# Kernel optimization log

Hardware: AMD Instinct MI355X
Metric: run time of the kernel (lower is better)

## Reference

```python
import jax, jax.numpy as jnp
import numpy as np

B, T, D, HS = 4, 2048, 1024, 64

def setup_inputs() -> dict:
    key = jax.random.key(0)
    kx, kk, kq, kv = jax.random.split(key, 4)
    scale = 1.0 / np.sqrt(D)
    return {
        "x": jax.random.normal(kx, (B, T, D), dtype=jnp.float32),
        "Wk": jax.random.normal(kk, (D, HS), dtype=jnp.float32) * scale,
        "Wq": jax.random.normal(kq, (D, HS), dtype=jnp.float32) * scale,
        "Wv": jax.random.normal(kv, (D, HS), dtype=jnp.float32) * scale,
    }

def reference(x, Wk, Wq, Wv):
    # x: [B, T, D]; projections to [B, T, HS]
    k = jnp.einsum("btd,dh->bth", x, Wk)
    q = jnp.einsum("btd,dh->bth", x, Wq)
    v = jnp.einsum("btd,dh->bth", x, Wv)
    # scores [B, T, T]; NOTE: original multiplies by sqrt(head_size) (faithful)
    att = jnp.einsum("bth,bsh->bts", q, k) * jnp.sqrt(jnp.float32(k.shape[-1]))
    Tq = x.shape[1]
    causal = jnp.tril(jnp.ones((Tq, Tq), dtype=bool))
    att = jnp.where(causal[None, :, :], att, -jnp.inf)
    p = jax.nn.softmax(att, axis=-1)
    # dropout = identity (eval mode)
    return jnp.einsum("bts,bsh->bth", p, v)
```

## Files before the change

### kernel.cpp

```cpp
#include <hip/hip_runtime.h>

#define Bn 4
#define Tn 2048
#define Dn 1024
#define HSn 64

typedef __attribute__((ext_vector_type(8))) short bf16x8;
typedef __attribute__((ext_vector_type(4))) float f32x4;
typedef __attribute__((ext_vector_type(4))) short s16x4;
typedef unsigned short u16;
typedef unsigned int u32;

__device__ __forceinline__ u16 f2bf_rne(float x) {
    u32 u = __float_as_uint(x);
    return (u16)((u + 0x7FFFu + ((u >> 16) & 1u)) >> 16);
}
__device__ __forceinline__ u16 f2bf_trunc(float x) {
    return (u16)(__float_as_uint(x) >> 16);
}
__device__ __forceinline__ float bf2f(u16 h) {
    return __uint_as_float(((u32)h) << 16);
}

#define GLL16(g, l)                                                        \
    __builtin_amdgcn_global_load_lds(                                      \
        (const __attribute__((address_space(1))) void*)(g),                \
        (__attribute__((address_space(3))) void*)(l), 16, 0, 0)

__global__ __launch_bounds__(256) void wprep_kernel(
    const float* __restrict__ Wk, const float* __restrict__ Wq,
    const float* __restrict__ Wv, u16* __restrict__ wtp)
{
    __shared__ float ws_[64][65];
    const int kb = blockIdx.x;
    const int w  = blockIdx.y;
    const float* __restrict__ W = (w == 0) ? Wk : (w == 1) ? Wq : Wv;
    const float scale = (w == 1) ? 8.0f : 1.0f;
    const int t = threadIdx.x;

    {
        const int kl = t >> 2, hq = t & 3;
        #pragma unroll
        for (int i = 0; i < 4; ++i) {
            float4 f = *(const float4*)(W + (size_t)(kb * 64 + kl) * 64 + hq * 16 + i * 4);
            ws_[kl][hq * 16 + i * 4 + 0] = f.x; ws_[kl][hq * 16 + i * 4 + 1] = f.y;
            ws_[kl][hq * 16 + i * 4 + 2] = f.z; ws_[kl][hq * 16 + i * 4 + 3] = f.w;
        }
    }
    __syncthreads();

    const int h = t & 63, quarter = t >> 6;
    const int n = w * 64 + h;
    const int ks = kb * 2 + (quarter >> 1);
    const int k_in0 = (quarter & 1) * 16;
    u16 hib[16], lob[16];
    #pragma unroll
    for (int j = 0; j < 16; ++j) {
        float v = ws_[quarter * 16 + j][h] * scale;
        u16 hi = f2bf_trunc(v);
        hib[j] = hi;
        lob[j] = f2bf_trunc(v - bf2f(hi));
    }
    u16* dst = wtp + (size_t)n * 2048 + ks * 64;
    *(uint4*)(dst + k_in0)          = *(const uint4*)&hib[0];
    *(uint4*)(dst + k_in0 + 8)      = *(const uint4*)&hib[8];
    *(uint4*)(dst + 32 + k_in0)     = *(const uint4*)&lob[0];
    *(uint4*)(dst + 32 + k_in0 + 8) = *(const uint4*)&lob[8];
}

#define NKS 32
#define XB(P) (smem + (P) * 4096)
#define BB(P) (smem + 12288 + (P) * 12288)

__global__ __launch_bounds__(256) void proj_gemm(
    const float* __restrict__ x, const u16* __restrict__ wtp,
    u16* __restrict__ qh8, u16* __restrict__ ql8,
    u16* __restrict__ kth, u16* __restrict__ ktl,
    u16* __restrict__ vtt)
{
    __shared__ __align__(16) unsigned char smem[49152];

    const int tid  = threadIdx.x;
    const int wave = tid >> 6, lane = tid & 63;
    const int lo4  = lane & 15, g = lane >> 4;
    const int ch   = blockIdx.x >> 8;
    const int row0 = (blockIdx.x & 255) * 32;
    const int rt   = wave >> 1;
    const int cbase = (wave & 1) * 3;
    const int rl = rt * 16 + lo4;
    const int wcol0 = ch * 96;

    f32x4 acc[3];
    #pragma unroll
    for (int c = 0; c < 3; ++c) acc[c] = (f32x4){0.f, 0.f, 0.f, 0.f};

    const int xr = tid >> 3, xc = tid & 7;
    const int xsw = (xc ^ (xr & 7)) << 2;
    const float* xsrc0 = x + (size_t)(row0 + xr) * Dn + xsw;

    #define STAGE(P, KS)                                                     \
        {                                                                    \
            GLL16(xsrc0 + (KS) * 32, XB(P) + tid * 16);                      \
            _Pragma("unroll")                                                \
            for (int i = 0; i < 3; ++i) {                                    \
                const int c = i * 256 + tid;                                 \
                const int n_ = c >> 3, p_ = c & 7;                           \
                const int l_ = p_ ^ (n_ & 7);                                \
                const u16* src = wtp + (size_t)(wcol0 + n_) * 2048 + (KS) * 64 \
                                 + ((l_ & 3) << 3) + ((l_ >> 2) << 5);       \
                GLL16(src, BB(P) + c * 16);                                  \
            }                                                                \
        }

    #define COMPUTE(P, KS)                                                   \
        {                                                                    \
            bf16x8 ah, al;                                                   \
            {                                                                \
                const unsigned char* xb = XB(P) + rl * 128;                  \
                f32x4 f0 = *(const f32x4*)(xb + (((2 * g + 0) ^ (rl & 7)) << 4)); \
                f32x4 f1 = *(const f32x4*)(xb + (((2 * g + 1) ^ (rl & 7)) << 4)); \
                _Pragma("unroll")                                            \
                for (int jj = 0; jj < 4; ++jj) {                             \
                    u16 h0 = f2bf_trunc(f0[jj]);                             \
                    ah[jj] = (short)h0;                                      \
                    al[jj] = (short)f2bf_trunc(f0[jj] - bf2f(h0));           \
                    u16 h1 = f2bf_trunc(f1[jj]);                             \
                    ah[4 + jj] = (short)h1;                                  \
                    al[4 + jj] = (short)f2bf_trunc(f1[jj] - bf2f(h1));       \
                }                                                            \
            }                                                                \
            _Pragma("unroll")                                                \
            for (int ct = 0; ct < 3; ++ct) {                                 \
                const int n = (cbase + ct) * 16 + lo4;                       \
                const unsigned char* bb = BB(P) + n * 128;                   \
                bf16x8 bh = *(const bf16x8*)(bb + (((g)     ^ (n & 7)) << 4)); \
                bf16x8 bl = *(const bf16x8*)(bb + (((4 + g) ^ (n & 7)) << 4)); \
                acc[ct] = __builtin_amdgcn_mfma_f32_16x16x32_bf16(ah, bh, acc[ct], 0, 0, 0); \
                acc[ct] = __builtin_amdgcn_mfma_f32_16x16x32_bf16(al, bh, acc[ct], 0, 0, 0); \
                acc[ct] = __builtin_amdgcn_mfma_f32_16x16x32_bf16(ah, bl, acc[ct], 0, 0, 0); \
            }                                                                \
        }

    STAGE(0, 0)
    STAGE(1, 1)
    int pb = 0;
    for (int ks = 0; ks < NKS; ++ks) {
        if (ks == NKS - 1) {
            asm volatile("s_waitcnt vmcnt(0)" ::: "memory");
        } else {
            asm volatile("s_waitcnt vmcnt(4)" ::: "memory");
        }
        __builtin_amdgcn_s_barrier();
        asm volatile("" ::: "memory");

        int ps = pb + 2; if (ps >= 3) ps -= 3;
        if (ks + 2 < NKS) STAGE(ps, ks + 2)
        COMPUTE(pb, ks)
        pb = (pb == 2) ? 0 : pb + 1;
    }

    const int grow = row0 + rt * 16 + g * 4;
    const int bb_ = grow >> 11, tl = grow & 2047;
    #pragma unroll
    for (int ct = 0; ct < 3; ++ct) {
        const int n = wcol0 + (cbase + ct) * 16 + lo4;
        if (n < 64) {
            const int kch = n >> 5, gi = (n >> 3) & 3, e = n & 7;
            const size_t base = (size_t)bb_ * 131072
                + (size_t)(((((tl >> 4) * 2 + kch) * 4 + gi) * 16 + (tl & 15)) * 8 + e);
            #pragma unroll
            for (int reg = 0; reg < 4; ++reg) {
                float v = acc[ct][reg];
                u16 hi = f2bf_trunc(v);
                kth[base + reg * 8] = hi;
                ktl[base + reg * 8] = f2bf_trunc(v - bf2f(hi));
            }
        } else if (n < 128) {
            #pragma unroll
            for (int reg = 0; reg < 4; ++reg) {
                float v = acc[ct][reg];
                u16 hi = f2bf_trunc(v);
                qh8[(size_t)(grow + reg) * HSn + (n - 64)] = hi;
                ql8[(size_t)(grow + reg) * HSn + (n - 64)] = f2bf_trunc(v - bf2f(hi));
            }
        } else {
            const int h = n - 128;
            s16x4 pack;
            #pragma unroll
            for (int reg = 0; reg < 4; ++reg)
                pack[reg] = (short)f2bf_rne(acc[ct][reg]);
            const size_t vidx = (size_t)bb_ * 131072
                + (size_t)((tl >> 5) * 2048 + (h >> 4) * 512 + (h & 15) * 32
                           + ((tl >> 3) & 3) * 8 + (tl & 7));
            *(s16x4*)(vtt + vidx) = pack;
        }
    }
}

struct KVset {
    bf16x8 kh0[2], kh1[2], kl0[2], kl1[2], vf[4];
};

__global__ __launch_bounds__(256, 2) void attn_kernel(
    const u16* __restrict__ qh8, const u16* __restrict__ ql8,
    const u16* __restrict__ kth, const u16* __restrict__ ktl,
    const u16* __restrict__ vtt, float* __restrict__ out)
{
    __shared__ __align__(16) unsigned char pbuf[4096];
    __shared__ __align__(16) float om_s[4][16][64];
    __shared__ float ml_s[4][16][2];

    const int tid  = threadIdx.x;
    const int wave = tid >> 6, lane = tid & 63;
    const int lo4  = lane & 15, g = lane >> 4;

    const int sblk = blockIdx.x >> 8, c = blockIdx.x & 255;
    const int tb = sblk ? 127 - (c >> 1) : (c >> 1);
    const int b  = 2 * sblk + (c & 1);
    const int t0 = tb * 16;

    const u16* qhp = qh8 + ((size_t)b * Tn + t0) * HSn;
    const u16* qlp = ql8 + ((size_t)b * Tn + t0) * HSn;
    const u16* kthb = kth + (size_t)b * 131072;
    const u16* ktlb = ktl + (size_t)b * 131072;
    const u16* vttb = vtt + (size_t)b * 131072;
    const int klane = lane * 8;
    const int vlane = lo4 * 32 + g * 8;

    bf16x8 qfh[2], qfl[2];
    #pragma unroll
    for (int ch = 0; ch < 2; ++ch) {
        qfh[ch] = *(const bf16x8*)(qhp + lo4 * HSn + ch * 32 + g * 8);
        qfl[ch] = *(const bf16x8*)(qlp + lo4 * HSn + ch * 32 + g * 8);
    }

    bf16x8 vones;
    #pragma unroll
    for (int i = 0; i < 8; ++i) vones[i] = (short)0x3F80;

    f32x4 O[4];
    #pragma unroll
    for (int n = 0; n < 4; ++n) O[n] = (f32x4){0.f, 0.f, 0.f, 0.f};
    float mrow[4], lrow[4];
    #pragma unroll
    for (int r = 0; r < 4; ++r) { mrow[r] = -1e30f; lrow[r] = 0.f; }

    const int nt = (t0 + 15) / 32 + 1;
    unsigned char* myPB = pbuf + wave * 1024;

    #define LOADSET(S, J)                                                     \
        {                                                                     \
            const u16* kb_ = kthb + (size_t)(2 * (J)) * 1024 + klane;         \
            const u16* lb_ = ktlb + (size_t)(2 * (J)) * 1024 + klane;         \
            S.kh0[0] = *(const bf16x8*)(kb_);                                 \
            S.kh1[0] = *(const bf16x8*)(kb_ + 512);                           \
            S.kh0[1] = *(const bf16x8*)(kb_ + 1024);                          \
            S.kh1[1] = *(const bf16x8*)(kb_ + 1536);                          \
            S.kl0[0] = *(const bf16x8*)(lb_);                                 \
            S.kl1[0] = *(const bf16x8*)(lb_ + 512);                           \
            S.kl0[1] = *(const bf16x8*)(lb_ + 1024);                          \
            S.kl1[1] = *(const bf16x8*)(lb_ + 1536);                          \
            const u16* vb_ = vttb + (size_t)(J) * 2048 + vlane;               \
            S.vf[0] = *(const bf16x8*)(vb_);                                  \
            S.vf[1] = *(const bf16x8*)(vb_ + 512);                            \
            S.vf[2] = *(const bf16x8*)(vb_ + 1024);                           \
            S.vf[3] = *(const bf16x8*)(vb_ + 1536);                           \
        }

    #define COMPUTE_ATT(S, J)                                                 \
        {                                                                     \
            const int s0 = (J) * 32;                                          \
            f32x4 accS[2];                                                    \
            __builtin_amdgcn_s_setprio(1);                                    \
            _Pragma("unroll")                                                 \
            for (int sb = 0; sb < 2; ++sb) {                                  \
                f32x4 a = (f32x4){0.f, 0.f, 0.f, 0.f};                        \
                a = __builtin_amdgcn_mfma_f32_16x16x32_bf16(qfh[0], S.kh0[sb], a, 0, 0, 0); \
                a = __builtin_amdgcn_mfma_f32_16x16x32_bf16(qfh[1], S.kh1[sb], a, 0, 0, 0); \
                a = __builtin_amdgcn_mfma_f32_16x16x32_bf16(qfl[0], S.kh0[sb], a, 0, 0, 0); \
                a = __builtin_amdgcn_mfma_f32_16x16x32_bf16(qfl[1], S.kh1[sb], a, 0, 0, 0); \
                a = __builtin_amdgcn_mfma_f32_16x16x32_bf16(qfh[0], S.kl0[sb], a, 0, 0, 0); \
                a = __builtin_amdgcn_mfma_f32_16x16x32_bf16(qfh[1], S.kl1[sb], a, 0, 0, 0); \
                accS[sb] = a;                                                 \
            }                                                                 \
            __builtin_amdgcn_s_setprio(0);                                    \
            float v0s[4], v1s[4], mts[4];                                     \
            _Pragma("unroll")                                                 \
            for (int reg = 0; reg < 4; ++reg) {                               \
                const int tg  = t0 + g * 4 + reg;                             \
                v0s[reg] = (s0 + lo4      <= tg) ? accS[0][reg] : -1e30f;     \
                v1s[reg] = (s0 + 16 + lo4 <= tg) ? accS[1][reg] : -1e30f;     \
                float mt = fmaxf(v0s[reg], v1s[reg]);                         \
                mt = fmaxf(mt, __shfl_xor(mt, 1));                            \
                mt = fmaxf(mt, __shfl_xor(mt, 2));                            \
                mt = fmaxf(mt, __shfl_xor(mt, 4));                            \
                mt = fmaxf(mt, __shfl_xor(mt, 8));                            \
                mts[reg] = mt;                                                \
            }                                                                 \
            const bool grew = (mts[0] > mrow[0]) | (mts[1] > mrow[1])         \
                            | (mts[2] > mrow[2]) | (mts[3] > mrow[3]);        \
            if (__any(grew)) {                                                \
                _Pragma("unroll")                                             \
                for (int reg = 0; reg < 4; ++reg) {                           \
                    float mn = fmaxf(mrow[reg], mts[reg]);                    \
                    float alpha = __expf(mrow[reg] - mn);                     \
                    lrow[reg] *= alpha;                                       \
                    mrow[reg] = mn;                                           \
                    _Pragma("unroll")                                         \
                    for (int n = 0; n < 4; ++n) O[n][reg] *= alpha;           \
                }                                                             \
            }                                                                 \
            _Pragma("unroll")                                                 \
            for (int reg = 0; reg < 4; ++reg) {                               \
                const int tg  = t0 + g * 4 + reg;                             \
                float p0 = (s0 + lo4      <= tg) ? __expf(v0s[reg] - mrow[reg]) : 0.f; \
                float p1 = (s0 + 16 + lo4 <= tg) ? __expf(v1s[reg] - mrow[reg]) : 0.f; \
                const int irow = g * 4 + reg;                                 \
                *(u16*)(myPB + ((irow * 64 + lo4 * 2) ^ (reg << 4)))      = f2bf_rne(p0); \
                *(u16*)(myPB + ((irow * 64 + 32 + lo4 * 2) ^ (reg << 4))) = f2bf_rne(p1); \
            }                                                                 \
            bf16x8 pf = *(const bf16x8*)(myPB + ((lo4 * 64 + 16 * g) ^ ((lo4 & 3) << 4))); \
            __builtin_amdgcn_s_setprio(1);                                    \
            f32x4 lacc = (f32x4){0.f, 0.f, 0.f, 0.f};                         \
            lacc = __builtin_amdgcn_mfma_f32_16x16x32_bf16(pf, vones, lacc, 0, 0, 0); \
            _Pragma("unroll")                                                 \
            for (int n = 0; n < 4; ++n)                                       \
                O[n] = __builtin_amdgcn_mfma_f32_16x16x32_bf16(pf, S.vf[n], O[n], 0, 0, 0); \
            __builtin_amdgcn_s_setprio(0);                                    \
            _Pragma("unroll")                                                 \
            for (int reg = 0; reg < 4; ++reg) lrow[reg] += lacc[reg];         \
        }

    KVset A, B;
    int j = wave;
    if (j < nt) LOADSET(A, j)
    while (j < nt) {
        if (j + 4 < nt) LOADSET(B, j + 4)
        COMPUTE_ATT(A, j)
        if (j + 4 < nt) {
            if (j + 8 < nt) LOADSET(A, j + 8)
            COMPUTE_ATT(B, j + 4)
        }
        j += 8;
    }

    #pragma unroll
    for (int n = 0; n < 4; ++n)
        #pragma unroll
        for (int reg = 0; reg < 4; ++reg)
            om_s[wave][g * 4 + reg][n * 16 + lo4] = O[n][reg];
    if (lo4 == 0) {
        #pragma unroll
        for (int reg = 0; reg < 4; ++reg) {
            ml_s[wave][g * 4 + reg][0] = mrow[reg];
            ml_s[wave][g * 4 + reg][1] = lrow[reg];
        }
    }
    __syncthreads();

    const int r  = tid >> 4;
    const int h4 = (tid & 15) * 4;
    float mw[4], lw[4], mstar = -1e30f;
    #pragma unroll
    for (int w = 0; w < 4; ++w) {
        mw[w] = ml_s[w][r][0];
        lw[w] = ml_s[w][r][1];
        mstar = fmaxf(mstar, mw[w]);
    }
    float lstar = 0.f, ew[4];
    #pragma unroll
    for (int w = 0; w < 4; ++w) { ew[w] = __expf(mw[w] - mstar); lstar += lw[w] * ew[w]; }
    float4 a4 = {0.f, 0.f, 0.f, 0.f};
    #pragma unroll
    for (int w = 0; w < 4; ++w) {
        float4 t4 = *(const float4*)&om_s[w][r][h4];
        a4.x += t4.x * ew[w]; a4.y += t4.y * ew[w];
        a4.z += t4.z * ew[w]; a4.w += t4.w * ew[w];
    }
    const float inv = 1.f / lstar;
    a4.x *= inv; a4.y *= inv; a4.z *= inv; a4.w *= inv;
    *(float4*)(out + ((size_t)b * Tn + t0 + r) * HSn + h4) = a4;
}

extern "C" void kernel_launch(void* const* d_in, const int* in_sizes, int n_in,
                              void* d_out, int out_size, void* d_ws, size_t ws_size,
                              hipStream_t stream) {
    const float* x  = (const float*)d_in[0];
    const float* Wk = (const float*)d_in[1];
    const float* Wq = (const float*)d_in[2];
    const float* Wv = (const float*)d_in[3];
    float* out = (float*)d_out;

    const size_t per = (size_t)Bn * Tn * HSn;
    u16* qh8 = (u16*)d_ws;
    u16* ql8 = qh8 + per;
    u16* kth = ql8 + per;
    u16* ktl = kth + per;
    u16* vtt = ktl + per;
    u16* wtp = vtt + per;

    hipLaunchKernelGGL(wprep_kernel, dim3(16, 3), dim3(256), 0, stream,
                       Wk, Wq, Wv, wtp);
    hipLaunchKernelGGL(proj_gemm, dim3(512), dim3(256), 0, stream,
                       x, wtp, qh8, ql8, kth, ktl, vtt);
    hipLaunchKernelGGL(attn_kernel, dim3(512), dim3(256), 0, stream,
                       qh8, ql8, kth, ktl, vtt, out);
}
```

Baseline: 45.88 us.

## Compute all projection columns per block to reuse converted x tiles

Each proj_gemm block now covers all 192 Q/K/V output columns for its 32 rows instead of half of them, so the grid shrinks from 512 to 256 blocks. Each wave handles both 16-row subtiles across three column tiles, reusing the hi/lo bf16 conversion of x and the loaded weight fragments. This avoids loading and splitting each x tile twice, at the cost of a much larger LDS footprint (weights buffer doubled), more accumulator registers, and fewer blocks for latency hiding.

```diff
diff --git a/kernel.cpp b/kernel.cpp
--- a/kernel.cpp
+++ b/kernel.cpp
@@ -70,7 +70,7 @@
 
 #define NKS 32
 #define XB(P) (smem + (P) * 4096)
-#define BB(P) (smem + 12288 + (P) * 12288)
+#define BB(P) (smem + 12288 + (P) * 24576)
 
 __global__ __launch_bounds__(256) void proj_gemm(
     const float* __restrict__ x, const u16* __restrict__ wtp,
@@ -78,21 +78,19 @@
     u16* __restrict__ kth, u16* __restrict__ ktl,
     u16* __restrict__ vtt)
 {
-    __shared__ __align__(16) unsigned char smem[49152];
+    __shared__ __align__(16) unsigned char smem[86016];
 
     const int tid  = threadIdx.x;
     const int wave = tid >> 6, lane = tid & 63;
     const int lo4  = lane & 15, g = lane >> 4;
-    const int ch   = blockIdx.x >> 8;
-    const int row0 = (blockIdx.x & 255) * 32;
-    const int rt   = wave >> 1;
-    const int cbase = (wave & 1) * 3;
-    const int rl = rt * 16 + lo4;
-    const int wcol0 = ch * 96;
-
-    f32x4 acc[3];
-    #pragma unroll
-    for (int c = 0; c < 3; ++c) acc[c] = (f32x4){0.f, 0.f, 0.f, 0.f};
+    const int row0 = blockIdx.x * 32;
+    const int cbase = wave * 3;
+
+    f32x4 acc[2][3];
+    #pragma unroll
+    for (int r2 = 0; r2 < 2; ++r2)
+        #pragma unroll
+        for (int c = 0; c < 3; ++c) acc[r2][c] = (f32x4){0.f, 0.f, 0.f, 0.f};
 
     const int xr = tid >> 3, xc = tid & 7;
     const int xsw = (xc ^ (xr & 7)) << 2;
@@ -102,11 +100,11 @@
         {                                                                    \
             GLL16(xsrc0 + (KS) * 32, XB(P) + tid * 16);                      \
             _Pragma("unroll")                                                \
-            for (int i = 0; i < 3; ++i) {                                    \
+            for (int i = 0; i < 6; ++i) {                                    \
                 const int c = i * 256 + tid;                                 \
                 const int n_ = c >> 3, p_ = c & 7;                           \
                 const int l_ = p_ ^ (n_ & 7);                                \
-                const u16* src = wtp + (size_t)(wcol0 + n_) * 2048 + (KS) * 64 \
+                const u16* src = wtp + (size_t)n_ * 2048 + (KS) * 64         \
                                  + ((l_ & 3) << 3) + ((l_ >> 2) << 5);       \
                 GLL16(src, BB(P) + c * 16);                                  \
             }                                                                \
@@ -114,19 +112,21 @@
 
     #define COMPUTE(P, KS)                                                   \
         {                                                                    \
-            bf16x8 ah, al;                                                   \
-            {                                                                \
-                const unsigned char* xb = XB(P) + rl * 128;                  \
-                f32x4 f0 = *(const f32x4*)(xb + (((2 * g + 0) ^ (rl & 7)) << 4)); \
-                f32x4 f1 = *(const f32x4*)(xb + (((2 * g + 1) ^ (rl & 7)) << 4)); \
+            bf16x8 ah[2], al[2];                                             \
+            _Pragma("unroll")                                                \
+            for (int r2 = 0; r2 < 2; ++r2) {                                 \
+                const int rl2 = r2 * 16 + lo4;                               \
+                const unsigned char* xb = XB(P) + rl2 * 128;                 \
+                f32x4 f0 = *(const f32x4*)(xb + (((2 * g + 0) ^ (rl2 & 7)) << 4)); \
+                f32x4 f1 = *(const f32x4*)(xb + (((2 * g + 1) ^ (rl2 & 7)) << 4)); \
                 _Pragma("unroll")                                            \
                 for (int jj = 0; jj < 4; ++jj) {                             \
                     u16 h0 = f2bf_trunc(f0[jj]);                             \
-                    ah[jj] = (short)h0;                                      \
-                    al[jj] = (short)f2bf_trunc(f0[jj] - bf2f(h0));           \
+                    ah[r2][jj] = (short)h0;                                  \
+                    al[r2][jj] = (short)f2bf_trunc(f0[jj] - bf2f(h0));       \
                     u16 h1 = f2bf_trunc(f1[jj]);                             \
-                    ah[4 + jj] = (short)h1;                                  \
-                    al[4 + jj] = (short)f2bf_trunc(f1[jj] - bf2f(h1));       \
+                    ah[r2][4 + jj] = (short)h1;                              \
+                    al[r2][4 + jj] = (short)f2bf_trunc(f1[jj] - bf2f(h1));   \
                 }                                                            \
             }                                                                \
             _Pragma("unroll")                                                \
@@ -135,9 +135,12 @@
                 const unsigned char* bb = BB(P) + n * 128;                   \
                 bf16x8 bh = *(const bf16x8*)(bb + (((g)     ^ (n & 7)) << 4)); \
                 bf16x8 bl = *(const bf16x8*)(bb + (((4 + g) ^ (n & 7)) << 4)); \
-                acc[ct] = __builtin_amdgcn_mfma_f32_16x16x32_bf16(ah, bh, acc[ct], 0, 0, 0); \
-                acc[ct] = __builtin_amdgcn_mfma_f32_16x16x32_bf16(al, bh, acc[ct], 0, 0, 0); \
-                acc[ct] = __builtin_amdgcn_mfma_f32_16x16x32_bf16(ah, bl, acc[ct], 0, 0, 0); \
+                _Pragma("unroll")                                            \
+                for (int r2 = 0; r2 < 2; ++r2) {                             \
+                    acc[r2][ct] = __builtin_amdgcn_mfma_f32_16x16x32_bf16(ah[r2], bh, acc[r2][ct], 0, 0, 0); \
+                    acc[r2][ct] = __builtin_amdgcn_mfma_f32_16x16x32_bf16(al[r2], bh, acc[r2][ct], 0, 0, 0); \
+                    acc[r2][ct] = __builtin_amdgcn_mfma_f32_16x16x32_bf16(ah[r2], bl, acc[r2][ct], 0, 0, 0); \
+                }                                                            \
             }                                                                \
         }
 
@@ -148,7 +151,7 @@
         if (ks == NKS - 1) {
             asm volatile("s_waitcnt vmcnt(0)" ::: "memory");
         } else {
-            asm volatile("s_waitcnt vmcnt(4)" ::: "memory");
+            asm volatile("s_waitcnt vmcnt(7)" ::: "memory");
         }
         __builtin_amdgcn_s_barrier();
         asm volatile("" ::: "memory");
@@ -159,40 +162,43 @@
         pb = (pb == 2) ? 0 : pb + 1;
     }
 
-    const int grow = row0 + rt * 16 + g * 4;
-    const int bb_ = grow >> 11, tl = grow & 2047;
-    #pragma unroll
-    for (int ct = 0; ct < 3; ++ct) {
-        const int n = wcol0 + (cbase + ct) * 16 + lo4;
-        if (n < 64) {
-            const int kch = n >> 5, gi = (n >> 3) & 3, e = n & 7;
-            const size_t base = (size_t)bb_ * 131072
-                + (size_t)(((((tl >> 4) * 2 + kch) * 4 + gi) * 16 + (tl & 15)) * 8 + e);
-            #pragma unroll
-            for (int reg = 0; reg < 4; ++reg) {
-                float v = acc[ct][reg];
-                u16 hi = f2bf_trunc(v);
-                kth[base + reg * 8] = hi;
-                ktl[base + reg * 8] = f2bf_trunc(v - bf2f(hi));
+    #pragma unroll
+    for (int r2 = 0; r2 < 2; ++r2) {
+        const int grow = row0 + r2 * 16 + g * 4;
+        const int bb_ = grow >> 11, tl = grow & 2047;
+        #pragma unroll
+        for (int ct = 0; ct < 3; ++ct) {
+            const int n = (cbase + ct) * 16 + lo4;
+            if (n < 64) {
+                const int kch = n >> 5, gi = (n >> 3) & 3, e = n & 7;
+                const size_t base = (size_t)bb_ * 131072
+                    + (size_t)(((((tl >> 4) * 2 + kch) * 4 + gi) * 16 + (tl & 15)) * 8 + e);
+                #pragma unroll
+                for (int reg = 0; reg < 4; ++reg) {
+                    float v = acc[r2][ct][reg];
+                    u16 hi = f2bf_trunc(v);
+                    kth[base + reg * 8] = hi;
+                    ktl[base + reg * 8] = f2bf_trunc(v - bf2f(hi));
+                }
+            } else if (n < 128) {
+                #pragma unroll
+                for (int reg = 0; reg < 4; ++reg) {
+                    float v = acc[r2][ct][reg];
+                    u16 hi = f2bf_trunc(v);
+                    qh8[(size_t)(grow + reg) * HSn + (n - 64)] = hi;
+                    ql8[(size_t)(grow + reg) * HSn + (n - 64)] = f2bf_trunc(v - bf2f(hi));
+                }
+            } else {
+                const int h = n - 128;
+                s16x4 pack;
+                #pragma unroll
+                for (int reg = 0; reg < 4; ++reg)
+                    pack[reg] = (short)f2bf_rne(acc[r2][ct][reg]);
+                const size_t vidx = (size_t)bb_ * 131072
+                    + (size_t)((tl >> 5) * 2048 + (h >> 4) * 512 + (h & 15) * 32
+                               + ((tl >> 3) & 3) * 8 + (tl & 7));
+                *(s16x4*)(vtt + vidx) = pack;
             }
-        } else if (n < 128) {
-            #pragma unroll
-            for (int reg = 0; reg < 4; ++reg) {
-                float v = acc[ct][reg];
-                u16 hi = f2bf_trunc(v);
-                qh8[(size_t)(grow + reg) * HSn + (n - 64)] = hi;
-                ql8[(size_t)(grow + reg) * HSn + (n - 64)] = f2bf_trunc(v - bf2f(hi));
-            }
-        } else {
-            const int h = n - 128;
-            s16x4 pack;
-            #pragma unroll
-            for (int reg = 0; reg < 4; ++reg)
-                pack[reg] = (short)f2bf_rne(acc[ct][reg]);
-            const size_t vidx = (size_t)bb_ * 131072
-                + (size_t)((tl >> 5) * 2048 + (h >> 4) * 512 + (h & 15) * 32
-                           + ((tl >> 3) & 3) * 8 + (tl & 7));
-            *(s16x4*)(vtt + vidx) = pack;
         }
     }
 }
@@ -401,7 +407,7 @@
 
     hipLaunchKernelGGL(wprep_kernel, dim3(16, 3), dim3(256), 0, stream,
                        Wk, Wq, Wv, wtp);
-    hipLaunchKernelGGL(proj_gemm, dim3(512), dim3(256), 0, stream,
+    hipLaunchKernelGGL(proj_gemm, dim3(256), dim3(256), 0, stream,
                        x, wtp, qh8, ql8, kth, ktl, vtt);
     hipLaunchKernelGGL(attn_kernel, dim3(512), dim3(256), 0, stream,
                        qh8, ql8, kth, ktl, vtt, out);
```

After: 50.51 us. 1.1x slower.

## Pre-swizzle weights into MFMA fragment layout and load them directly to registers

Applied to the files above, without the earlier changes.

The weight-prep kernel now writes the bf16 hi/lo weights already arranged in per-lane MFMA fragment order. The projection GEMM reads these fragments straight from global memory into registers, double-buffered across k-steps, instead of staging them through LDS. x is now staged in larger 128-wide chunks with one barrier per chunk rather than one per 32-wide step, and MFMA issue is wrapped in s_setprio. This cuts LDS traffic and barrier count, at the cost of more register pressure and global-load latency that is exposed unless the register prefetch hides it.

```diff
diff --git a/kernel.cpp b/kernel.cpp
--- a/kernel.cpp
+++ b/kernel.cpp
@@ -29,7 +29,7 @@
 
 __global__ __launch_bounds__(256) void wprep_kernel(
     const float* __restrict__ Wk, const float* __restrict__ Wq,
-    const float* __restrict__ Wv, u16* __restrict__ wtp)
+    const float* __restrict__ Wv, u16* __restrict__ wtp2)
 {
     __shared__ float ws_[64][65];
     const int kb = blockIdx.x;
@@ -50,9 +50,8 @@
     __syncthreads();
 
     const int h = t & 63, quarter = t >> 6;
-    const int n = w * 64 + h;
-    const int ks = kb * 2 + (quarter >> 1);
-    const int k_in0 = (quarter & 1) * 16;
+    const int nt = w * 4 + (h >> 4);
+    const int ksub = quarter >> 1;
     u16 hib[16], lob[16];
     #pragma unroll
     for (int j = 0; j < 16; ++j) {
@@ -61,34 +60,35 @@
         hib[j] = hi;
         lob[j] = f2bf_trunc(v - bf2f(hi));
     }
-    u16* dst = wtp + (size_t)n * 2048 + ks * 64;
-    *(uint4*)(dst + k_in0)          = *(const uint4*)&hib[0];
-    *(uint4*)(dst + k_in0 + 8)      = *(const uint4*)&hib[8];
-    *(uint4*)(dst + 32 + k_in0)     = *(const uint4*)&lob[0];
-    *(uint4*)(dst + 32 + k_in0 + 8) = *(const uint4*)&lob[8];
-}
-
-#define NKS 32
-#define XB(P) (smem + (P) * 4096)
-#define BB(P) (smem + 12288 + (P) * 12288)
+    const int lane0 = ((quarter * 2 + 0) & 3) * 16 + (h & 15);
+    const int lane1 = ((quarter * 2 + 1) & 3) * 16 + (h & 15);
+    u16* base = wtp2 + (size_t)kb * 24576 + (size_t)(ksub * 12 + nt) * 1024;
+    *(uint4*)(base + lane0 * 8)       = *(const uint4*)&hib[0];
+    *(uint4*)(base + lane1 * 8)       = *(const uint4*)&hib[8];
+    *(uint4*)(base + 512 + lane0 * 8) = *(const uint4*)&lob[0];
+    *(uint4*)(base + 512 + lane1 * 8) = *(const uint4*)&lob[8];
+}
+
+struct Bset { bf16x8 bh[3], bl[3]; };
 
 __global__ __launch_bounds__(256) void proj_gemm(
-    const float* __restrict__ x, const u16* __restrict__ wtp,
+    const float* __restrict__ x, const u16* __restrict__ wtp2,
     u16* __restrict__ qh8, u16* __restrict__ ql8,
     u16* __restrict__ kth, u16* __restrict__ ktl,
     u16* __restrict__ vtt)
 {
-    __shared__ __align__(16) unsigned char smem[49152];
+    __shared__ __align__(16) unsigned char smem[32768];
 
     const int tid  = threadIdx.x;
     const int wave = tid >> 6, lane = tid & 63;
     const int lo4  = lane & 15, g = lane >> 4;
-    const int ch   = blockIdx.x >> 8;
+    const int chh  = blockIdx.x >> 8;
     const int row0 = (blockIdx.x & 255) * 32;
     const int rt   = wave >> 1;
-    const int cbase = (wave & 1) * 3;
-    const int rl = rt * 16 + lo4;
-    const int wcol0 = ch * 96;
+    const int cg   = wave & 1;
+    const int rl   = rt * 16 + lo4;
+    const int wcol0 = chh * 96;
+    const int ntbase = chh * 6 + cg * 3;
 
     f32x4 acc[3];
     #pragma unroll
@@ -97,73 +97,75 @@
     const int xr = tid >> 3, xc = tid & 7;
     const int xsw = (xc ^ (xr & 7)) << 2;
     const float* xsrc0 = x + (size_t)(row0 + xr) * Dn + xsw;
-
-    #define STAGE(P, KS)                                                     \
+    const u16* bp0 = wtp2 + (size_t)ntbase * 1024 + lane * 8;
+
+    #define XSTAGE(P, W_)                                                    \
         {                                                                    \
-            GLL16(xsrc0 + (KS) * 32, XB(P) + tid * 16);                      \
             _Pragma("unroll")                                                \
-            for (int i = 0; i < 3; ++i) {                                    \
-                const int c = i * 256 + tid;                                 \
-                const int n_ = c >> 3, p_ = c & 7;                           \
-                const int l_ = p_ ^ (n_ & 7);                                \
-                const u16* src = wtp + (size_t)(wcol0 + n_) * 2048 + (KS) * 64 \
-                                 + ((l_ & 3) << 3) + ((l_ >> 2) << 5);       \
-                GLL16(src, BB(P) + c * 16);                                  \
-            }                                                                \
-        }
-
-    #define COMPUTE(P, KS)                                                   \
+            for (int s_ = 0; s_ < 4; ++s_)                                   \
+                GLL16(xsrc0 + (W_) * 128 + s_ * 32,                          \
+                      smem + (P) * 16384 + s_ * 4096 + tid * 16);            \
+        }
+
+    #define LOADB(S, KS)                                                     \
         {                                                                    \
-            bf16x8 ah, al;                                                   \
-            {                                                                \
-                const unsigned char* xb = XB(P) + rl * 128;                  \
-                f32x4 f0 = *(const f32x4*)(xb + (((2 * g + 0) ^ (rl & 7)) << 4)); \
-                f32x4 f1 = *(const f32x4*)(xb + (((2 * g + 1) ^ (rl & 7)) << 4)); \
-                _Pragma("unroll")                                            \
-                for (int jj = 0; jj < 4; ++jj) {                             \
-                    u16 h0 = f2bf_trunc(f0[jj]);                             \
-                    ah[jj] = (short)h0;                                      \
-                    al[jj] = (short)f2bf_trunc(f0[jj] - bf2f(h0));           \
-                    u16 h1 = f2bf_trunc(f1[jj]);                             \
-                    ah[4 + jj] = (short)h1;                                  \
-                    al[4 + jj] = (short)f2bf_trunc(f1[jj] - bf2f(h1));       \
-                }                                                            \
-            }                                                                \
+            const u16* bp = bp0 + (size_t)(KS) * 12288;                      \
             _Pragma("unroll")                                                \
             for (int ct = 0; ct < 3; ++ct) {                                 \
-                const int n = (cbase + ct) * 16 + lo4;                       \
-                const unsigned char* bb = BB(P) + n * 128;                   \
-                bf16x8 bh = *(const bf16x8*)(bb + (((g)     ^ (n & 7)) << 4)); \
-                bf16x8 bl = *(const bf16x8*)(bb + (((4 + g) ^ (n & 7)) << 4)); \
-                acc[ct] = __builtin_amdgcn_mfma_f32_16x16x32_bf16(ah, bh, acc[ct], 0, 0, 0); \
-                acc[ct] = __builtin_amdgcn_mfma_f32_16x16x32_bf16(al, bh, acc[ct], 0, 0, 0); \
-                acc[ct] = __builtin_amdgcn_mfma_f32_16x16x32_bf16(ah, bl, acc[ct], 0, 0, 0); \
+                S.bh[ct] = *(const bf16x8*)(bp + ct * 1024);                 \
+                S.bl[ct] = *(const bf16x8*)(bp + ct * 1024 + 512);           \
             }                                                                \
         }
 
-    STAGE(0, 0)
-    STAGE(1, 1)
-    int pb = 0;
-    for (int ks = 0; ks < NKS; ++ks) {
-        if (ks == NKS - 1) {
-            asm volatile("s_waitcnt vmcnt(0)" ::: "memory");
-        } else {
-            asm volatile("s_waitcnt vmcnt(4)" ::: "memory");
-        }
-        __builtin_amdgcn_s_barrier();
-        asm volatile("" ::: "memory");
-
-        int ps = pb + 2; if (ps >= 3) ps -= 3;
-        if (ks + 2 < NKS) STAGE(ps, ks + 2)
-        COMPUTE(pb, ks)
-        pb = (pb == 2) ? 0 : pb + 1;
+    #define KSTEP(P, S_, SET)                                                \
+        {                                                                    \
+            const unsigned char* xb = smem + (P) * 16384 + (S_) * 4096 + rl * 128; \
+            f32x4 f0 = *(const f32x4*)(xb + (((2 * g + 0) ^ (rl & 7)) << 4)); \
+            f32x4 f1 = *(const f32x4*)(xb + (((2 * g + 1) ^ (rl & 7)) << 4)); \
+            bf16x8 ah, al;                                                   \
+            _Pragma("unroll")                                                \
+            for (int jj = 0; jj < 4; ++jj) {                                 \
+                u16 h0 = f2bf_trunc(f0[jj]);                                 \
+                ah[jj] = (short)h0;                                          \
+                al[jj] = (short)f2bf_trunc(f0[jj] - bf2f(h0));               \
+                u16 h1 = f2bf_trunc(f1[jj]);                                 \
+                ah[4 + jj] = (short)h1;                                      \
+                al[4 + jj] = (short)f2bf_trunc(f1[jj] - bf2f(h1));           \
+            }                                                                \
+            __builtin_amdgcn_s_setprio(1);                                   \
+            _Pragma("unroll")                                                \
+            for (int ct = 0; ct < 3; ++ct) {                                 \
+                acc[ct] = __builtin_amdgcn_mfma_f32_16x16x32_bf16(ah, SET.bh[ct], acc[ct], 0, 0, 0); \
+                acc[ct] = __builtin_amdgcn_mfma_f32_16x16x32_bf16(al, SET.bh[ct], acc[ct], 0, 0, 0); \
+                acc[ct] = __builtin_amdgcn_mfma_f32_16x16x32_bf16(ah, SET.bl[ct], acc[ct], 0, 0, 0); \
+            }                                                                \
+            __builtin_amdgcn_s_setprio(0);                                   \
+        }
+
+    Bset BA, BB;
+    XSTAGE(0, 0)
+    LOADB(BA, 0)
+    __syncthreads();
+
+    for (int w = 0; w < 8; ++w) {
+        const int P = w & 1;
+        if (w + 1 < 8) XSTAGE(P ^ 1, w + 1)
+        #pragma unroll
+        for (int s = 0; s < 4; s += 2) {
+            const int ks = w * 4 + s;
+            if (ks + 1 < 32) LOADB(BB, ks + 1)
+            KSTEP(P, s, BA)
+            if (ks + 2 < 32) LOADB(BA, ks + 2)
+            KSTEP(P, s + 1, BB)
+        }
+        __syncthreads();
     }
 
     const int grow = row0 + rt * 16 + g * 4;
     const int bb_ = grow >> 11, tl = grow & 2047;
     #pragma unroll
     for (int ct = 0; ct < 3; ++ct) {
-        const int n = wcol0 + (cbase + ct) * 16 + lo4;
+        const int n = wcol0 + (cg * 3 + ct) * 16 + lo4;
         if (n < 64) {
             const int kch = n >> 5, gi = (n >> 3) & 3, e = n & 7;
             const size_t base = (size_t)bb_ * 131072
@@ -397,12 +399,12 @@
     u16* kth = ql8 + per;
     u16* ktl = kth + per;
     u16* vtt = ktl + per;
-    u16* wtp = vtt + per;
+    u16* wtp2 = vtt + per;
 
     hipLaunchKernelGGL(wprep_kernel, dim3(16, 3), dim3(256), 0, stream,
-                       Wk, Wq, Wv, wtp);
+                       Wk, Wq, Wv, wtp2);
     hipLaunchKernelGGL(proj_gemm, dim3(512), dim3(256), 0, stream,
-                       x, wtp, qh8, ql8, kth, ktl, vtt);
+                       x, wtp2, qh8, ql8, kth, ktl, vtt);
     hipLaunchKernelGGL(attn_kernel, dim3(512), dim3(256), 0, stream,
                        qh8, ql8, kth, ktl, vtt, out);
 }
```

Result: slower. 48.27 us (+5.2%).

## Double proj_gemm row tile to 64 with 512-thread blocks sharing weight tiles

Applied to the files above, without the earlier changes.

The projection GEMM now gives each block 64 rows of x (8 waves) instead of 32 rows (4 waves), so every staged weight tile in shared memory feeds twice as many rows. The grid is halved to 256 blocks and shared memory grows to 60KB across three stages, with per-thread wait counts adjusted because threads now issue different numbers of async loads. This cuts redundant weight loads from global memory, at the cost of fewer blocks (lower occupancy and less latency hiding) and uneven load issue across threads.

```diff
diff --git a/kernel.cpp b/kernel.cpp
--- a/kernel.cpp
+++ b/kernel.cpp
@@ -69,26 +69,26 @@
 }
 
 #define NKS 32
-#define XB(P) (smem + (P) * 4096)
-#define BB(P) (smem + 12288 + (P) * 12288)
-
-__global__ __launch_bounds__(256) void proj_gemm(
+#define XB(P) (smem + (P) * 20480)
+#define BB(P) (smem + (P) * 20480 + 8192)
+
+__global__ __launch_bounds__(512) void proj_gemm(
     const float* __restrict__ x, const u16* __restrict__ wtp,
     u16* __restrict__ qh8, u16* __restrict__ ql8,
     u16* __restrict__ kth, u16* __restrict__ ktl,
     u16* __restrict__ vtt)
 {
-    __shared__ __align__(16) unsigned char smem[49152];
+    __shared__ __align__(16) unsigned char smem[61440];
 
     const int tid  = threadIdx.x;
     const int wave = tid >> 6, lane = tid & 63;
     const int lo4  = lane & 15, g = lane >> 4;
-    const int ch   = blockIdx.x >> 8;
-    const int row0 = (blockIdx.x & 255) * 32;
+    const int chh  = blockIdx.x >> 7;
+    const int row0 = (blockIdx.x & 127) * 64;
     const int rt   = wave >> 1;
-    const int cbase = (wave & 1) * 3;
-    const int rl = rt * 16 + lo4;
-    const int wcol0 = ch * 96;
+    const int cg   = wave & 1;
+    const int rl   = rt * 16 + lo4;
+    const int wcol0 = chh * 96;
 
     f32x4 acc[3];
     #pragma unroll
@@ -101,9 +101,16 @@
     #define STAGE(P, KS)                                                     \
         {                                                                    \
             GLL16(xsrc0 + (KS) * 32, XB(P) + tid * 16);                      \
-            _Pragma("unroll")                                                \
-            for (int i = 0; i < 3; ++i) {                                    \
-                const int c = i * 256 + tid;                                 \
+            {                                                                \
+                const int c = tid;                                           \
+                const int n_ = c >> 3, p_ = c & 7;                           \
+                const int l_ = p_ ^ (n_ & 7);                                \
+                const u16* src = wtp + (size_t)(wcol0 + n_) * 2048 + (KS) * 64 \
+                                 + ((l_ & 3) << 3) + ((l_ >> 2) << 5);       \
+                GLL16(src, BB(P) + c * 16);                                  \
+            }                                                                \
+            if (tid < 256) {                                                 \
+                const int c = 512 + tid;                                     \
                 const int n_ = c >> 3, p_ = c & 7;                           \
                 const int l_ = p_ ^ (n_ & 7);                                \
                 const u16* src = wtp + (size_t)(wcol0 + n_) * 2048 + (KS) * 64 \
@@ -131,10 +138,10 @@
             }                                                                \
             _Pragma("unroll")                                                \
             for (int ct = 0; ct < 3; ++ct) {                                 \
-                const int n = (cbase + ct) * 16 + lo4;                       \
-                const unsigned char* bb = BB(P) + n * 128;                   \
-                bf16x8 bh = *(const bf16x8*)(bb + (((g)     ^ (n & 7)) << 4)); \
-                bf16x8 bl = *(const bf16x8*)(bb + (((4 + g) ^ (n & 7)) << 4)); \
+                const int nloc = (cg * 3 + ct) * 16 + lo4;                   \
+                const unsigned char* bb = BB(P) + nloc * 128;                \
+                bf16x8 bh = *(const bf16x8*)(bb + (((g)     ^ (nloc & 7)) << 4)); \
+                bf16x8 bl = *(const bf16x8*)(bb + (((4 + g) ^ (nloc & 7)) << 4)); \
                 acc[ct] = __builtin_amdgcn_mfma_f32_16x16x32_bf16(ah, bh, acc[ct], 0, 0, 0); \
                 acc[ct] = __builtin_amdgcn_mfma_f32_16x16x32_bf16(al, bh, acc[ct], 0, 0, 0); \
                 acc[ct] = __builtin_amdgcn_mfma_f32_16x16x32_bf16(ah, bl, acc[ct], 0, 0, 0); \
@@ -147,8 +154,10 @@
     for (int ks = 0; ks < NKS; ++ks) {
         if (ks == NKS - 1) {
             asm volatile("s_waitcnt vmcnt(0)" ::: "memory");
+        } else if (tid < 256) {
+            asm volatile("s_waitcnt vmcnt(3)" ::: "memory");
         } else {
-            asm volatile("s_waitcnt vmcnt(4)" ::: "memory");
+            asm volatile("s_waitcnt vmcnt(2)" ::: "memory");
         }
         __builtin_amdgcn_s_barrier();
         asm volatile("" ::: "memory");
@@ -163,7 +172,7 @@
     const int bb_ = grow >> 11, tl = grow & 2047;
     #pragma unroll
     for (int ct = 0; ct < 3; ++ct) {
-        const int n = wcol0 + (cbase + ct) * 16 + lo4;
+        const int n = wcol0 + (cg * 3 + ct) * 16 + lo4;
         if (n < 64) {
             const int kch = n >> 5, gi = (n >> 3) & 3, e = n & 7;
             const size_t base = (size_t)bb_ * 131072
@@ -401,7 +410,7 @@
 
     hipLaunchKernelGGL(wprep_kernel, dim3(16, 3), dim3(256), 0, stream,
                        Wk, Wq, Wv, wtp);
-    hipLaunchKernelGGL(proj_gemm, dim3(512), dim3(256), 0, stream,
+    hipLaunchKernelGGL(proj_gemm, dim3(256), dim3(512), 0, stream,
                        x, wtp, qh8, ql8, kth, ktl, vtt);
     hipLaunchKernelGGL(attn_kernel, dim3(512), dim3(256), 0, stream,
                        qh8, ql8, kth, ktl, vtt, out);
```

New measurement: 46.18 us. About the same (+0.7%).
